# Kernel optimization log

Measured on AMD Instinct MI355X. Metric: run time of the kernel, lower is better.

The kernel has to match this reference:

```python
import jax, jax.numpy as jnp
import numpy as np

DIM = 64
HEADS = 4
N_NODES = 50000
N_EDGES = 800000
NEG_SLOPE = 0.2


def setup_inputs() -> dict:
    key = jax.random.key(0)
    k1, k2, k3, k4, k5 = jax.random.split(key, 5)
    meta_x = jax.random.normal(k1, (N_NODES, DIM), dtype=jnp.float32)
    meta_edge_index = jax.random.randint(k2, (2, N_EDGES), 0, N_NODES, dtype=jnp.int64)
    # GATConv params: shared source/dest Linear (no bias), per-head attention vecs, output bias.
    glorot = float(np.sqrt(2.0 / (DIM + HEADS * DIM)))
    W = jax.random.normal(k3, (DIM, HEADS * DIM), dtype=jnp.float32) * glorot  # x @ W
    att_src = jax.random.normal(k4, (1, HEADS, DIM), dtype=jnp.float32) * glorot
    att_dst = jax.random.normal(k5, (1, HEADS, DIM), dtype=jnp.float32) * glorot
    bias = jnp.zeros((DIM,), dtype=jnp.float32)
    return {"meta_x": meta_x, "meta_edge_index": meta_edge_index,
            "W": W, "att_src": att_src, "att_dst": att_dst, "bias": bias}


def reference(meta_x, meta_edge_index, W, att_src, att_dst, bias):
    N = meta_x.shape[0]
    # PyG GATConv default: add self-loops
    loops = jnp.arange(N, dtype=meta_edge_index.dtype)
    edge = jnp.concatenate([meta_edge_index, jnp.stack([loops, loops])], axis=1)
    src, dst = edge[0], edge[1]

    x = (meta_x @ W).reshape(N, HEADS, DIM)            # [N, H, C]
    a_src = jnp.sum(x * att_src, axis=-1)              # [N, H]
    a_dst = jnp.sum(x * att_dst, axis=-1)              # [N, H]

    logits = a_src[src] + a_dst[dst]                   # [E, H]
    logits = jax.nn.leaky_relu(logits, NEG_SLOPE)

    # segment softmax over edges grouped by destination node
    seg_max = jax.ops.segment_max(logits, dst, num_segments=N)   # [N, H]
    ex = jnp.exp(logits - seg_max[dst])
    seg_sum = jax.ops.segment_sum(ex, dst, num_segments=N)
    alpha = ex / (seg_sum[dst] + 1e-16)                # [E, H]

    msg = x[src] * alpha[:, :, None]                   # [E, H, C]
    out = jax.ops.segment_sum(msg, dst, num_segments=N)  # [N, H, C]
    # concat=False -> mean over heads, then bias
    return out.mean(axis=1) + bias
```

## Files before the change

### kernel.cpp

```cpp
#include <hip/hip_runtime.h>
#include <math.h>

#define MAXDEG 64

__device__ __forceinline__ float lrelu(float v) { return v > 0.0f ? v : 0.2f * v; }

__global__ void patt_kernel(const float* __restrict__ W, const float* __restrict__ att_src,
                            const float* __restrict__ att_dst, float* __restrict__ wsrc,
                            float* __restrict__ wdst) {
  int t = threadIdx.x;
  int h = t >> 6, k = t & 63;
  const float* wrow = W + (size_t)k * 256 + h * 64;
  const float* as = att_src + h * 64;
  const float* ad = att_dst + h * 64;
  float ss = 0.f, sd = 0.f;
#pragma unroll
  for (int c = 0; c < 64; ++c) {
    float w = wrow[c];
    ss = fmaf(w, as[c], ss);
    sd = fmaf(w, ad[c], sd);
  }
  wsrc[k * 4 + h] = ss;
  wdst[k * 4 + h] = sd;
}

__global__ void nattn_kernel(const float* __restrict__ x, const float4* __restrict__ wsrc4,
                             const float4* __restrict__ wdst4, float4* __restrict__ asrc4,
                             float4* __restrict__ adst4, int N) {
  int lane = threadIdx.x & 63;
  int n = blockIdx.x * 4 + (threadIdx.x >> 6);
  if (n >= N) return;
  float xv = x[(size_t)n * 64 + lane];
  float4 ws = wsrc4[lane], wd = wdst4[lane];
  float s0 = xv * ws.x, s1 = xv * ws.y, s2 = xv * ws.z, s3 = xv * ws.w;
  float d0 = xv * wd.x, d1 = xv * wd.y, d2 = xv * wd.z, d3 = xv * wd.w;
#pragma unroll
  for (int m = 1; m < 64; m <<= 1) {
    s0 += __shfl_xor(s0, m, 64); s1 += __shfl_xor(s1, m, 64);
    s2 += __shfl_xor(s2, m, 64); s3 += __shfl_xor(s3, m, 64);
    d0 += __shfl_xor(d0, m, 64); d1 += __shfl_xor(d1, m, 64);
    d2 += __shfl_xor(d2, m, 64); d3 += __shfl_xor(d3, m, 64);
  }
  if (lane == 0) {
    asrc4[n] = make_float4(s0, s1, s2, s3);
    adst4[n] = make_float4(d0, d1, d2, d3);
  }
}

__global__ void hist_kernel(const int* __restrict__ ei, int* __restrict__ counts,
                            int E, int N) {
  int e = blockIdx.x * 256 + threadIdx.x;
  int ET = E + N;
  if (e >= ET) return;
  int dst = (e < E) ? ei[(size_t)E + e] : (e - E);
  atomicAdd(&counts[dst], 1);
}

__global__ void scatter_kernel(const int* __restrict__ ei, int* __restrict__ cursor,
                               int* __restrict__ src_sorted, int E, int N) {
  int e = blockIdx.x * 256 + threadIdx.x;
  int ET = E + N;
  if (e >= ET) return;
  int src, dst;
  if (e < E) {
    src = ei[e];
    dst = ei[(size_t)E + e];
  } else {
    src = dst = e - E;
  }
  int pos = atomicAdd(&cursor[dst], 1);
  src_sorted[pos] = src;
}

__global__ void hist4_kernel(const int* __restrict__ ei, int* __restrict__ counts,
                             int E, int N) {
  int i = blockIdx.x * 256 + threadIdx.x;
  int E4 = E >> 2;
  if (i < E4) {
    int4 d = ((const int4*)(ei + E))[i];
    atomicAdd(&counts[d.x], 1);
    atomicAdd(&counts[d.y], 1);
    atomicAdd(&counts[d.z], 1);
    atomicAdd(&counts[d.w], 1);
  } else if (i < E4 + N) {
    atomicAdd(&counts[i - E4], 1);
  }
}

__global__ void scatter4_kernel(const int* __restrict__ ei, int* __restrict__ cursor,
                                int* __restrict__ srt, int E, int N) {
  int i = blockIdx.x * 256 + threadIdx.x;
  int E4 = E >> 2;
  if (i < E4) {
    int4 s4 = ((const int4*)ei)[i];
    int4 d4 = ((const int4*)(ei + E))[i];
    int p;
    p = atomicAdd(&cursor[d4.x], 1); srt[p] = s4.x;
    p = atomicAdd(&cursor[d4.y], 1); srt[p] = s4.y;
    p = atomicAdd(&cursor[d4.z], 1); srt[p] = s4.z;
    p = atomicAdd(&cursor[d4.w], 1); srt[p] = s4.w;
  } else if (i < E4 + N) {
    int node = i - E4;
    int p = atomicAdd(&cursor[node], 1);
    srt[p] = node;
  }
}

__global__ void scanA_kernel(const int* __restrict__ cnt, int* __restrict__ tsum, int N) {
  int b = blockIdx.x, t = threadIdx.x;
  int idx = b * 256 + t;
  int v = (idx < N) ? cnt[idx] : 0;
#pragma unroll
  for (int m = 1; m < 64; m <<= 1) v += __shfl_xor(v, m, 64);
  __shared__ int ws[4];
  if ((t & 63) == 0) ws[t >> 6] = v;
  __syncthreads();
  if (t == 0) tsum[b] = ws[0] + ws[1] + ws[2] + ws[3];
}

__global__ void scanB_kernel(int* __restrict__ tsum, int ntiles) {
  __shared__ int part[256];
  int t = threadIdx.x;
  int carry = 0;
  for (int b0 = 0; b0 < ntiles; b0 += 256) {
    int idx = b0 + t;
    int v = (idx < ntiles) ? tsum[idx] : 0;
    part[t] = v;
    __syncthreads();
    for (int d = 1; d < 256; d <<= 1) {
      int u = (t >= d) ? part[t - d] : 0;
      __syncthreads();
      part[t] += u;
      __syncthreads();
    }
    if (idx < ntiles) tsum[idx] = part[t] - v + carry;
    carry += part[255];
    __syncthreads();
  }
}

__global__ void scanC_kernel(const int* __restrict__ cnt, const int* __restrict__ tsum,
                             int* __restrict__ row, int* __restrict__ cur, int N) {
  __shared__ int part[256];
  int b = blockIdx.x, t = threadIdx.x;
  int idx = b * 256 + t;
  int c = (idx < N) ? cnt[idx] : 0;
  part[t] = c;
  __syncthreads();
  for (int d = 1; d < 256; d <<= 1) {
    int u = (t >= d) ? part[t - d] : 0;
    __syncthreads();
    part[t] += u;
    __syncthreads();
  }
  int exc = part[t] - c + tsum[b];
  if (idx < N) {
    row[idx] = exc;
    cur[idx] = exc;
    if (idx == N - 1) row[N] = exc + c;
  }
}

__global__ __launch_bounds__(256) void agg_kernel(
    const int* __restrict__ srt, const int* __restrict__ row,
    const float4* __restrict__ asrc4, const float4* __restrict__ adst4,
    const float* __restrict__ x, float* __restrict__ agg, int N) {
  __shared__ float4 alL[4][MAXDEG];
  __shared__ int slL[4][MAXDEG];
  int t = threadIdx.x, w = t >> 6, lane = t & 63;
  int n = blockIdx.x * 4 + w;
  if (n >= N) return;
  int start = row[n], end = row[n + 1];
  int deg = end - start;
  float4 ad = adst4[n];
  float t0 = 0.f, t1 = 0.f, t2 = 0.f, t3 = 0.f;
  if (deg <= MAXDEG) {
    for (int b = 0; b < deg; b += 64) {
      if (b + lane < deg) {
        int sl = srt[start + b + lane];
        float4 as = asrc4[sl];
        float4 e;
        e.x = __expf(lrelu(as.x + ad.x));
        e.y = __expf(lrelu(as.y + ad.y));
        e.z = __expf(lrelu(as.z + ad.z));
        e.w = __expf(lrelu(as.w + ad.w));
        alL[w][b + lane] = e;
        slL[w][b + lane] = sl;
        t0 += e.x; t1 += e.y; t2 += e.z; t3 += e.w;
      }
    }
  } else {
    for (int b = start; b < end; b += 64) {
      int idx = b + lane;
      if (idx < end) {
        int sl = srt[idx];
        float4 as = asrc4[sl];
        t0 += __expf(lrelu(as.x + ad.x));
        t1 += __expf(lrelu(as.y + ad.y));
        t2 += __expf(lrelu(as.z + ad.z));
        t3 += __expf(lrelu(as.w + ad.w));
      }
    }
  }
#pragma unroll
  for (int m = 1; m < 64; m <<= 1) {
    t0 += __shfl_xor(t0, m, 64);
    t1 += __shfl_xor(t1, m, 64);
    t2 += __shfl_xor(t2, m, 64);
    t3 += __shfl_xor(t3, m, 64);
  }
  float r0 = 0.25f / (t0 + 1e-16f), r1 = 0.25f / (t1 + 1e-16f);
  float r2 = 0.25f / (t2 + 1e-16f), r3 = 0.25f / (t3 + 1e-16f);
  float a0 = 0.f, a1 = 0.f, a2 = 0.f, a3 = 0.f;
  if (deg <= MAXDEG) {
    int j = 0;
    for (; j + 4 <= deg; j += 4) {
      float4 e0 = alL[w][j], e1 = alL[w][j + 1], e2 = alL[w][j + 2], e3 = alL[w][j + 3];
      int q0 = slL[w][j], q1 = slL[w][j + 1], q2 = slL[w][j + 2], q3 = slL[w][j + 3];
      float v0 = x[(size_t)q0 * 64 + lane];
      float v1 = x[(size_t)q1 * 64 + lane];
      float v2 = x[(size_t)q2 * 64 + lane];
      float v3 = x[(size_t)q3 * 64 + lane];
      a0 = fmaf(e0.x, v0, a0); a1 = fmaf(e0.y, v0, a1);
      a2 = fmaf(e0.z, v0, a2); a3 = fmaf(e0.w, v0, a3);
      a0 = fmaf(e1.x, v1, a0); a1 = fmaf(e1.y, v1, a1);
      a2 = fmaf(e1.z, v1, a2); a3 = fmaf(e1.w, v1, a3);
      a0 = fmaf(e2.x, v2, a0); a1 = fmaf(e2.y, v2, a1);
      a2 = fmaf(e2.z, v2, a2); a3 = fmaf(e2.w, v2, a3);
      a0 = fmaf(e3.x, v3, a0); a1 = fmaf(e3.y, v3, a1);
      a2 = fmaf(e3.z, v3, a2); a3 = fmaf(e3.w, v3, a3);
    }
    for (; j < deg; ++j) {
      float4 e0 = alL[w][j];
      int q0 = slL[w][j];
      float v0 = x[(size_t)q0 * 64 + lane];
      a0 = fmaf(e0.x, v0, a0); a1 = fmaf(e0.y, v0, a1);
      a2 = fmaf(e0.z, v0, a2); a3 = fmaf(e0.w, v0, a3);
    }
  } else {
    for (int b = start; b < end; b += 64) {
      int cnt = end - b;
      if (cnt > 64) cnt = 64;
      int idx = b + lane;
      int sl = 0;
      float e0 = 0.f, e1 = 0.f, e2 = 0.f, e3 = 0.f;
      if (idx < end) {
        sl = srt[idx];
        float4 as = asrc4[sl];
        e0 = __expf(lrelu(as.x + ad.x));
        e1 = __expf(lrelu(as.y + ad.y));
        e2 = __expf(lrelu(as.z + ad.z));
        e3 = __expf(lrelu(as.w + ad.w));
      }
      for (int j = 0; j < cnt; ++j) {
        int sj = __shfl(sl, j, 64);
        float b0 = __shfl(e0, j, 64), b1 = __shfl(e1, j, 64);
        float b2 = __shfl(e2, j, 64), b3 = __shfl(e3, j, 64);
        float v = x[(size_t)sj * 64 + lane];
        a0 = fmaf(b0, v, a0); a1 = fmaf(b1, v, a1);
        a2 = fmaf(b2, v, a2); a3 = fmaf(b3, v, a3);
      }
    }
  }
  float* ao = agg + (size_t)n * 256;
  ao[lane] = a0 * r0;
  ao[64 + lane] = a1 * r1;
  ao[128 + lane] = a2 * r2;
  ao[192 + lane] = a3 * r3;
}

__global__ __launch_bounds__(256) void proj_kernel(
    const float* __restrict__ agg, const float* __restrict__ W,
    const float* __restrict__ bias, float* __restrict__ out, int N) {
  __shared__ float aggL[4][256];
  __shared__ float pL[4][4][64];
  int t = threadIdx.x, w = t >> 6, lane = t & 63;
  float Wreg[64];
#pragma unroll
  for (int k = 0; k < 64; ++k) Wreg[k] = W[(size_t)k * 256 + w * 64 + lane];
  float bv = bias[lane];
  int ngroups = (N + 3) >> 2;
  for (int g = blockIdx.x; g < ngroups; g += gridDim.x) {
    int n0 = g * 4;
    __syncthreads();
    {
      int nn = n0 + w;
      if (nn < N)
        *(float4*)&aggL[w][(t & 63) * 4] =
            *(const float4*)&agg[(size_t)nn * 256 + (t & 63) * 4];
      else
        *(float4*)&aggL[w][(t & 63) * 4] = make_float4(0.f, 0.f, 0.f, 0.f);
    }
    __syncthreads();
    float acc0 = 0.f, acc1 = 0.f, acc2 = 0.f, acc3 = 0.f;
#pragma unroll
    for (int k4 = 0; k4 < 16; ++k4) {
      float4 av0 = *(const float4*)&aggL[0][w * 64 + k4 * 4];
      float4 av1 = *(const float4*)&aggL[1][w * 64 + k4 * 4];
      float4 av2 = *(const float4*)&aggL[2][w * 64 + k4 * 4];
      float4 av3 = *(const float4*)&aggL[3][w * 64 + k4 * 4];
      float w0 = Wreg[k4 * 4 + 0], w1 = Wreg[k4 * 4 + 1];
      float w2 = Wreg[k4 * 4 + 2], w3 = Wreg[k4 * 4 + 3];
      acc0 = fmaf(av0.x, w0, acc0); acc0 = fmaf(av0.y, w1, acc0);
      acc0 = fmaf(av0.z, w2, acc0); acc0 = fmaf(av0.w, w3, acc0);
      acc1 = fmaf(av1.x, w0, acc1); acc1 = fmaf(av1.y, w1, acc1);
      acc1 = fmaf(av1.z, w2, acc1); acc1 = fmaf(av1.w, w3, acc1);
      acc2 = fmaf(av2.x, w0, acc2); acc2 = fmaf(av2.y, w1, acc2);
      acc2 = fmaf(av2.z, w2, acc2); acc2 = fmaf(av2.w, w3, acc2);
      acc3 = fmaf(av3.x, w0, acc3); acc3 = fmaf(av3.y, w1, acc3);
      acc3 = fmaf(av3.z, w2, acc3); acc3 = fmaf(av3.w, w3, acc3);
    }
    pL[w][0][lane] = acc0;
    pL[w][1][lane] = acc1;
    pL[w][2][lane] = acc2;
    pL[w][3][lane] = acc3;
    __syncthreads();
    int nn = n0 + w;
    if (nn < N) {
      out[(size_t)nn * 64 + lane] = pL[0][w][lane] + pL[1][w][lane] +
                                    pL[2][w][lane] + pL[3][w][lane] + bv;
    }
  }
}

__global__ __launch_bounds__(256) void gatout_kernel(
    const int* __restrict__ srt, const int* __restrict__ row,
    const float4* __restrict__ asrc4, const float4* __restrict__ adst4,
    const float* __restrict__ x, const float* __restrict__ W,
    const float* __restrict__ bias, float* __restrict__ out, int N) {
  __shared__ float4 smem4[320];
  float4 (*alL)[MAXDEG] = (float4(*)[MAXDEG])smem4;
  int (*slL)[MAXDEG] = (int(*)[MAXDEG])(smem4 + 256);
  float (*buf)[4][64] = (float(*)[4][64])smem4;
  int t = threadIdx.x, w = t >> 6, lane = t & 63;
  float Wreg[64];
#pragma unroll
  for (int k = 0; k < 64; ++k) Wreg[k] = W[(size_t)k * 256 + w * 64 + lane];
  float bv = bias[lane];
  int ngroups = (N + 3) >> 2;
  for (int g = blockIdx.x; g < ngroups; g += gridDim.x) {
    int n = g * 4 + w;
    float a0 = 0.f, a1 = 0.f, a2 = 0.f, a3 = 0.f;
    float r0 = 0.f, r1 = 0.f, r2 = 0.f, r3 = 0.f;
    __syncthreads();
    if (n < N) {
      int start = row[n], end = row[n + 1];
      int deg = end - start;
      float4 ad = adst4[n];
      float t0 = 0.f, t1 = 0.f, t2 = 0.f, t3 = 0.f;
      if (deg <= MAXDEG) {
        for (int b = 0; b < deg; b += 64) {
          if (b + lane < deg) {
            int sl = srt[start + b + lane];
            float4 as = asrc4[sl];
            float4 e;
            e.x = __expf(lrelu(as.x + ad.x));
            e.y = __expf(lrelu(as.y + ad.y));
            e.z = __expf(lrelu(as.z + ad.z));
            e.w = __expf(lrelu(as.w + ad.w));
            alL[w][b + lane] = e;
            slL[w][b + lane] = sl;
            t0 += e.x; t1 += e.y; t2 += e.z; t3 += e.w;
          }
        }
      } else {
        for (int b = start; b < end; b += 64) {
          int idx = b + lane;
          if (idx < end) {
            int sl = srt[idx];
            float4 as = asrc4[sl];
            t0 += __expf(lrelu(as.x + ad.x));
            t1 += __expf(lrelu(as.y + ad.y));
            t2 += __expf(lrelu(as.z + ad.z));
            t3 += __expf(lrelu(as.w + ad.w));
          }
        }
      }
#pragma unroll
      for (int m = 1; m < 64; m <<= 1) {
        t0 += __shfl_xor(t0, m, 64);
        t1 += __shfl_xor(t1, m, 64);
        t2 += __shfl_xor(t2, m, 64);
        t3 += __shfl_xor(t3, m, 64);
      }
      r0 = 0.25f / (t0 + 1e-16f); r1 = 0.25f / (t1 + 1e-16f);
      r2 = 0.25f / (t2 + 1e-16f); r3 = 0.25f / (t3 + 1e-16f);
      if (deg <= MAXDEG) {
        int j = 0;
        for (; j + 4 <= deg; j += 4) {
          float4 e0 = alL[w][j], e1 = alL[w][j + 1], e2 = alL[w][j + 2], e3 = alL[w][j + 3];
          int q0 = slL[w][j], q1 = slL[w][j + 1], q2 = slL[w][j + 2], q3 = slL[w][j + 3];
          float v0 = x[(size_t)q0 * 64 + lane];
          float v1 = x[(size_t)q1 * 64 + lane];
          float v2 = x[(size_t)q2 * 64 + lane];
          float v3 = x[(size_t)q3 * 64 + lane];
          a0 = fmaf(e0.x, v0, a0); a1 = fmaf(e0.y, v0, a1);
          a2 = fmaf(e0.z, v0, a2); a3 = fmaf(e0.w, v0, a3);
          a0 = fmaf(e1.x, v1, a0); a1 = fmaf(e1.y, v1, a1);
          a2 = fmaf(e1.z, v1, a2); a3 = fmaf(e1.w, v1, a3);
          a0 = fmaf(e2.x, v2, a0); a1 = fmaf(e2.y, v2, a1);
          a2 = fmaf(e2.z, v2, a2); a3 = fmaf(e2.w, v2, a3);
          a0 = fmaf(e3.x, v3, a0); a1 = fmaf(e3.y, v3, a1);
          a2 = fmaf(e3.z, v3, a2); a3 = fmaf(e3.w, v3, a3);
        }
        for (; j < deg; ++j) {
          float4 e0 = alL[w][j];
          int q0 = slL[w][j];
          float v0 = x[(size_t)q0 * 64 + lane];
          a0 = fmaf(e0.x, v0, a0); a1 = fmaf(e0.y, v0, a1);
          a2 = fmaf(e0.z, v0, a2); a3 = fmaf(e0.w, v0, a3);
        }
      } else {
        for (int b = start; b < end; b += 64) {
          int cnt = end - b;
          if (cnt > 64) cnt = 64;
          int idx = b + lane;
          int sl = 0;
          float e0 = 0.f, e1 = 0.f, e2 = 0.f, e3 = 0.f;
          if (idx < end) {
            sl = srt[idx];
            float4 as = asrc4[sl];
            e0 = __expf(lrelu(as.x + ad.x));
            e1 = __expf(lrelu(as.y + ad.y));
            e2 = __expf(lrelu(as.z + ad.z));
            e3 = __expf(lrelu(as.w + ad.w));
          }
          for (int j = 0; j < cnt; ++j) {
            int sj = __shfl(sl, j, 64);
            float b0 = __shfl(e0, j, 64), b1 = __shfl(e1, j, 64);
            float b2 = __shfl(e2, j, 64), b3 = __shfl(e3, j, 64);
            float v = x[(size_t)sj * 64 + lane];
            a0 = fmaf(b0, v, a0); a1 = fmaf(b1, v, a1);
            a2 = fmaf(b2, v, a2); a3 = fmaf(b3, v, a3);
          }
        }
      }
    }
    __syncthreads();
    buf[w][0][lane] = a0 * r0;
    buf[w][1][lane] = a1 * r1;
    buf[w][2][lane] = a2 * r2;
    buf[w][3][lane] = a3 * r3;
    __syncthreads();
    float acc0 = 0.f, acc1 = 0.f, acc2 = 0.f, acc3 = 0.f;
#pragma unroll
    for (int k4 = 0; k4 < 16; ++k4) {
      float4 av0 = *(const float4*)&buf[0][w][k4 * 4];
      float4 av1 = *(const float4*)&buf[1][w][k4 * 4];
      float4 av2 = *(const float4*)&buf[2][w][k4 * 4];
      float4 av3 = *(const float4*)&buf[3][w][k4 * 4];
      float w0 = Wreg[k4 * 4 + 0], w1 = Wreg[k4 * 4 + 1];
      float w2 = Wreg[k4 * 4 + 2], w3 = Wreg[k4 * 4 + 3];
      acc0 = fmaf(av0.x, w0, acc0); acc0 = fmaf(av0.y, w1, acc0);
      acc0 = fmaf(av0.z, w2, acc0); acc0 = fmaf(av0.w, w3, acc0);
      acc1 = fmaf(av1.x, w0, acc1); acc1 = fmaf(av1.y, w1, acc1);
      acc1 = fmaf(av1.z, w2, acc1); acc1 = fmaf(av1.w, w3, acc1);
      acc2 = fmaf(av2.x, w0, acc2); acc2 = fmaf(av2.y, w1, acc2);
      acc2 = fmaf(av2.z, w2, acc2); acc2 = fmaf(av2.w, w3, acc2);
      acc3 = fmaf(av3.x, w0, acc3); acc3 = fmaf(av3.y, w1, acc3);
      acc3 = fmaf(av3.z, w2, acc3); acc3 = fmaf(av3.w, w3, acc3);
    }
    __syncthreads();
    buf[w][0][lane] = acc0;
    buf[w][1][lane] = acc1;
    buf[w][2][lane] = acc2;
    buf[w][3][lane] = acc3;
    __syncthreads();
    if (n < N) {
      out[(size_t)n * 64 + lane] = buf[0][w][lane] + buf[1][w][lane] +
                                   buf[2][w][lane] + buf[3][w][lane] + bv;
    }
  }
}

extern "C" void kernel_launch(void* const* d_in, const int* in_sizes, int n_in,
                              void* d_out, int out_size, void* d_ws, size_t ws_size,
                              hipStream_t stream) {
  const float* meta_x = (const float*)d_in[0];
  const int* ei = (const int*)d_in[1];
  const float* W = (const float*)d_in[2];
  const float* att_src = (const float*)d_in[3];
  const float* att_dst = (const float*)d_in[4];
  const float* bias = (const float*)d_in[5];
  float* out = (float*)d_out;

  int N = in_sizes[0] / 64;
  int E = in_sizes[1] / 2;
  int ET = E + N;

  char* ws = (char*)d_ws;
  size_t off = 0;
  auto alloc = [&](size_t bytes) {
    size_t o = off;
    off += (bytes + 255) & ~(size_t)255;
    return o;
  };
  size_t o_wsrc = alloc(64 * 4 * sizeof(float));
  size_t o_wdst = alloc(64 * 4 * sizeof(float));
  size_t o_asrc = alloc((size_t)N * 4 * sizeof(float));
  size_t o_adst = alloc((size_t)N * 4 * sizeof(float));
  size_t o_cnt = alloc((size_t)N * sizeof(int));
  size_t o_row = alloc(((size_t)N + 1) * sizeof(int));
  size_t o_cur = alloc((size_t)N * sizeof(int));
  size_t o_srt = alloc((size_t)ET * sizeof(int));
  size_t o_ts = alloc((((size_t)N + 255) / 256) * sizeof(int));
  size_t base_sz = off;
  size_t o_agg = alloc((size_t)N * 256 * sizeof(float));
  bool split = (ws_size >= off);
  (void)base_sz;

  float* wsrc = (float*)(ws + o_wsrc);
  float* wdst = (float*)(ws + o_wdst);
  float4* asrc4 = (float4*)(ws + o_asrc);
  float4* adst4 = (float4*)(ws + o_adst);
  int* cnt = (int*)(ws + o_cnt);
  int* row = (int*)(ws + o_row);
  int* cur = (int*)(ws + o_cur);
  int* srt = (int*)(ws + o_srt);
  int* tsum = (int*)(ws + o_ts);
  float* aggp = (float*)(ws + o_agg);

  hipMemsetAsync(cnt, 0, (size_t)N * sizeof(int), stream);

  patt_kernel<<<1, 256, 0, stream>>>(W, att_src, att_dst, wsrc, wdst);
  nattn_kernel<<<(N + 3) / 4, 256, 0, stream>>>(meta_x, (const float4*)wsrc,
                                                (const float4*)wdst, asrc4, adst4, N);
  if ((E & 3) == 0) {
    int nt4 = (E >> 2) + N;
    hist4_kernel<<<(nt4 + 255) / 256, 256, 0, stream>>>(ei, cnt, E, N);
  } else {
    hist_kernel<<<(ET + 255) / 256, 256, 0, stream>>>(ei, cnt, E, N);
  }
  int ntiles = (N + 255) / 256;
  scanA_kernel<<<ntiles, 256, 0, stream>>>(cnt, tsum, N);
  scanB_kernel<<<1, 256, 0, stream>>>(tsum, ntiles);
  scanC_kernel<<<ntiles, 256, 0, stream>>>(cnt, tsum, row, cur, N);
  if ((E & 3) == 0) {
    int nt4 = (E >> 2) + N;
    scatter4_kernel<<<(nt4 + 255) / 256, 256, 0, stream>>>(ei, cur, srt, E, N);
  } else {
    scatter_kernel<<<(ET + 255) / 256, 256, 0, stream>>>(ei, cur, srt, E, N);
  }
  if (split) {
    agg_kernel<<<(N + 3) / 4, 256, 0, stream>>>(srt, row, asrc4, adst4, meta_x, aggp, N);
    int ngroups = (N + 3) / 4;
    int pgrid = ngroups < 2048 ? ngroups : 2048;
    proj_kernel<<<pgrid, 256, 0, stream>>>(aggp, W, bias, out, N);
  } else {
    int ngroups = (N + 3) / 4;
    int ggrid = ngroups < 2048 ? ngroups : 2048;
    gatout_kernel<<<ggrid, 256, 0, stream>>>(srt, row, asrc4, adst4, meta_x, W, bias, out, N);
  }
}
```

Measured before the change: 209.4 us.

## Partition CSR scatter by destination range across eight block slices for locality

The edge scatter kernel now splits work into eight slices of destination-node ranges, each handled by a group of blocks that scan all edges in a grid-stride loop and only insert edges whose destination falls in their slice. The aim is to concentrate atomic cursor updates and srt writes into a smaller address range per block group, improving cache or L2 locality (possibly per XCD on the MI355X). In exchange, the destination indices are read eight times. The grid becomes a fixed 2048 blocks, with source indices loaded only when needed.

Measured after the change: 197.1 us. 1.06x faster.

```diff
diff --git a/kernel.cpp b/kernel.cpp
--- a/kernel.cpp
+++ b/kernel.cpp
@@ -87,22 +87,32 @@
   }
 }
 
-__global__ void scatter4_kernel(const int* __restrict__ ei, int* __restrict__ cursor,
+__global__ void scatter8_kernel(const int* __restrict__ ei, int* __restrict__ cursor,
                                 int* __restrict__ srt, int E, int N) {
-  int i = blockIdx.x * 256 + threadIdx.x;
+  int slice = blockIdx.x & 7;
+  int bid = blockIdx.x >> 3;
+  int nb = gridDim.x >> 3;
+  int chunk = (N + 7) >> 3;
+  int lo = slice * chunk;
+  int hi = lo + chunk; if (hi > N) hi = N;
   int E4 = E >> 2;
-  if (i < E4) {
-    int4 s4 = ((const int4*)ei)[i];
-    int4 d4 = ((const int4*)(ei + E))[i];
-    int p;
-    p = atomicAdd(&cursor[d4.x], 1); srt[p] = s4.x;
-    p = atomicAdd(&cursor[d4.y], 1); srt[p] = s4.y;
-    p = atomicAdd(&cursor[d4.z], 1); srt[p] = s4.z;
-    p = atomicAdd(&cursor[d4.w], 1); srt[p] = s4.w;
-  } else if (i < E4 + N) {
-    int node = i - E4;
-    int p = atomicAdd(&cursor[node], 1);
-    srt[p] = node;
+  const int4* s4p = (const int4*)ei;
+  const int4* d4p = (const int4*)(ei + E);
+  int stride = nb * 256;
+  for (int i = bid * 256 + threadIdx.x; i < E4; i += stride) {
+    int4 d4 = d4p[i];
+    bool bx = (d4.x >= lo && d4.x < hi), by = (d4.y >= lo && d4.y < hi);
+    bool bz = (d4.z >= lo && d4.z < hi), bw = (d4.w >= lo && d4.w < hi);
+    if (!(bx || by || bz || bw)) continue;
+    int4 s4 = s4p[i];
+    if (bx) { int p = atomicAdd(&cursor[d4.x], 1); srt[p] = s4.x; }
+    if (by) { int p = atomicAdd(&cursor[d4.y], 1); srt[p] = s4.y; }
+    if (bz) { int p = atomicAdd(&cursor[d4.z], 1); srt[p] = s4.z; }
+    if (bw) { int p = atomicAdd(&cursor[d4.w], 1); srt[p] = s4.w; }
+  }
+  for (int n = lo + bid * 256 + threadIdx.x; n < hi; n += stride) {
+    int p = atomicAdd(&cursor[n], 1);
+    srt[p] = n;
   }
 }
 
@@ -536,8 +546,7 @@
   scanB_kernel<<<1, 256, 0, stream>>>(tsum, ntiles);
   scanC_kernel<<<ntiles, 256, 0, stream>>>(cnt, tsum, row, cur, N);
   if ((E & 3) == 0) {
-    int nt4 = (E >> 2) + N;
-    scatter4_kernel<<<(nt4 + 255) / 256, 256, 0, stream>>>(ei, cur, srt, E, N);
+    scatter8_kernel<<<2048, 256, 0, stream>>>(ei, cur, srt, E, N);
   } else {
     scatter_kernel<<<(ET + 255) / 256, 256, 0, stream>>>(ei, cur, srt, E, N);
   }
```
